# Performance work log

Measured on AMD Instinct MI355X. Metric: run time of the kernel, lower is better.

The kernel has to match this reference:

```python
import jax, jax.numpy as jnp
import numpy as np

B, S, D, H = 4, 2048, 1024, 16  # batch, seq, n_embd, n_head
HD = D // H  # head size = 64


def setup_inputs() -> dict:
    key = jax.random.key(0)
    ks = jax.random.split(key, 5)
    s = 0.02
    return {
        "x": jax.random.normal(ks[0], (B, S, D), dtype=jnp.float32),
        "W_attn": jax.random.normal(ks[1], (D, 3 * D), dtype=jnp.float32) * s,
        "b_attn": jnp.zeros((3 * D,), dtype=jnp.float32),
        "W_proj": jax.random.normal(ks[2], (D, D), dtype=jnp.float32) * s,
        "b_proj": jnp.zeros((D,), dtype=jnp.float32),
    }


def reference(x, W_attn, b_attn, W_proj, b_proj):
    Bx, Sx, Dx = x.shape
    qkv = x @ W_attn + b_attn  # [B,S,3D]
    q, k, v = jnp.split(qkv, 3, axis=-1)
    # [B,H,S,hd]
    q = q.reshape(Bx, Sx, H, HD).transpose(0, 2, 1, 3)
    k = k.reshape(Bx, Sx, H, HD).transpose(0, 2, 1, 3)
    v = v.reshape(Bx, Sx, H, HD).transpose(0, 2, 1, 3)
    scale = 1.0 / jnp.sqrt(jnp.asarray(HD, dtype=x.dtype))
    att = jnp.einsum("bhqd,bhkd->bhqk", q, k) * scale  # [B,H,S,S]
    causal = jnp.tril(jnp.ones((Sx, Sx), dtype=bool))
    att = jnp.where(causal[None, None, :, :], att, jnp.asarray(-jnp.inf, dtype=att.dtype))
    att = jax.nn.softmax(att, axis=-1)
    y = jnp.einsum("bhqk,bhkd->bhqd", att, v)  # [B,H,S,hd]
    y = y.transpose(0, 2, 1, 3).reshape(Bx, Sx, Dx)
    return y @ W_proj + b_proj
```

## Files before the change

kernel.cpp:

```cpp
#include <hip/hip_runtime.h>
#include <math.h>

#define SEQ 2048
#define DIM 1024
#define NH 16
#define HD 64
#define QKV_LD 3072

typedef __attribute__((ext_vector_type(8))) __bf16 bf16x8;
typedef __attribute__((ext_vector_type(8))) unsigned short u16x8;
typedef __attribute__((ext_vector_type(4))) unsigned short u16x4;
typedef __attribute__((ext_vector_type(4))) float f32x4;

typedef unsigned int __attribute__((may_alias)) u32a;

__device__ __forceinline__ unsigned short f2b(float f) {
  unsigned int b = __builtin_bit_cast(unsigned int, f);
  return (unsigned short)((b + 0x7fffu + ((b >> 16) & 1u)) >> 16);
}

__device__ __forceinline__ void gload_lds16(const void* g, void* l) {
  __builtin_amdgcn_global_load_lds((const __attribute__((address_space(1))) void*)g,
                                   (__attribute__((address_space(3))) void*)l,
                                   16, 0, 0);
}

__device__ __forceinline__ bf16x8 ld_frag16(const unsigned short* p) {
  bf16x8 r;
  __builtin_memcpy(&r, __builtin_assume_aligned((void*)p, 16), 16);
  return r;
}

#define BARRIER_VM4()  asm volatile("s_waitcnt vmcnt(4)\ns_barrier" ::: "memory")
#define BARRIER_VM6()  asm volatile("s_waitcnt vmcnt(6)\ns_barrier" ::: "memory")
#define BARRIER_LGKM() asm volatile("s_waitcnt lgkmcnt(0)\ns_barrier" ::: "memory")
#define PH_BAR()       asm volatile("s_barrier" ::: "memory")
#define LGKM0()        asm volatile("s_waitcnt lgkmcnt(0)" ::: "memory")
#define ISSUE_FENCE()  asm volatile("" ::: "memory")


__device__ __forceinline__ void transpose_tile_256(
    const float* __restrict__ W, unsigned short* __restrict__ WT,
    int K, int N, int bx, int by, int tid) {
  __shared__ float tile[32][33];
  const int n0 = bx * 32, k0 = by * 32;
  const int tx = tid & 31, ty0 = tid >> 5;
#pragma unroll
  for (int r = 0; r < 4; ++r)
    tile[ty0 + r * 8][tx] = W[(size_t)(k0 + ty0 + r * 8) * N + n0 + tx];
  __syncthreads();
#pragma unroll
  for (int r = 0; r < 4; ++r)
    WT[(size_t)(n0 + ty0 + r * 8) * K + k0 + tx] = f2b(tile[tx][ty0 + r * 8]);
}

__global__ __launch_bounds__(256) void prep_kernel(
    const float* __restrict__ x, unsigned short* __restrict__ xb, int n,
    const float* __restrict__ Wa, unsigned short* __restrict__ WaT,
    const float* __restrict__ Wp, unsigned short* __restrict__ WpT) {
  const int bid = blockIdx.x;
  const int tid = threadIdx.x;
  if (bid < 8192) {
    const int i = (bid * 256 + tid) * 4;
    if (i >= n) return;
    float4 v = *(const float4*)(x + i);
    u16x4 o;
    o.x = f2b(v.x); o.y = f2b(v.y); o.z = f2b(v.z); o.w = f2b(v.w);
    *(u16x4*)(xb + i) = o;
  } else if (bid < 8192 + 3072) {
    const int t = bid - 8192;
    transpose_tile_256(Wa, WaT, DIM, 3 * DIM, t % 96, t / 96, tid);
  } else {
    const int t = bid - (8192 + 3072);
    transpose_tile_256(Wp, WpT, DIM, DIM, t % 32, t / 32, tid);
  }
}


template <int OUT_F32>
__global__ __launch_bounds__(512, 2) void gemm_bt_v4_kernel(
    const unsigned short* __restrict__ A,
    const unsigned short* __restrict__ BT,
    const float* __restrict__ bias,
    void* __restrict__ C, int M, int N, int K,
    int scale_cols, float scale_val) {
  __shared__ __align__(16) unsigned short As[3][256 * 64];
  __shared__ __align__(16) unsigned short Bs[3][128 * 64];

  const int tid = threadIdx.x;
  const int wave = tid >> 6;
  const int lane = tid & 63;
  const int quad = lane >> 4;
  const int l16 = lane & 15;
  const int r7 = l16 & 7;
  const int m0 = blockIdx.y * 256;
  const int n0 = blockIdx.x * 128;
  const int wm = (wave >> 1) * 64;
  const int wn = (wave & 1) * 64;

  const int srow = tid >> 3;
  const int sg = (tid & 7) ^ (srow & 7);
  const size_t a_gb = (size_t)(m0 + srow) * K + sg * 8;
  const size_t b_gb = (size_t)(n0 + srow) * K + sg * 8;

  f32x4 acc[4][4] = {};
  const int NT = K >> 6;

#define G_STAGE_A(kt_, buf_, j_)                                               \
  gload_lds16(A + a_gb + (size_t)(j_) * 64 * K + (size_t)(kt_) * 64,           \
              &As[buf_][(j_) * 4096 + wave * 512])
#define G_STAGE_B(kt_, buf_, j_)                                               \
  gload_lds16(BT + b_gb + (size_t)(j_) * 64 * K + (size_t)(kt_) * 64,          \
              &Bs[buf_][(j_) * 4096 + wave * 512])
#define G_STAGE_ALL(kt_, buf_)                                                 \
  {                                                                            \
    G_STAGE_A(kt_, buf_, 0); G_STAGE_A(kt_, buf_, 1);                          \
    G_STAGE_A(kt_, buf_, 2); G_STAGE_A(kt_, buf_, 3);                          \
    G_STAGE_B(kt_, buf_, 0); G_STAGE_B(kt_, buf_, 1);                          \
  }

#define V4_PHASE(kk_, la_, lb_, STAGES_, BAR_)                                 \
  {                                                                            \
    const int colg = ((((kk_) << 2) | quad) ^ r7) << 3;                        \
    bf16x8 af[4], bfr[4];                                                      \
    _Pragma("unroll") for (int i = 0; i < 4; ++i)                              \
      af[i] = ld_frag16(&(la_)[(wm + i * 16 + l16) * 64 + colg]);              \
    _Pragma("unroll") for (int i = 0; i < 4; ++i)                              \
      bfr[i] = ld_frag16(&(lb_)[(wn + i * 16 + l16) * 64 + colg]);             \
    STAGES_;                                                                   \
    BAR_;                                                                      \
    LGKM0();                                                                   \
    __builtin_amdgcn_s_setprio(1);                                             \
    _Pragma("unroll") for (int ni = 0; ni < 4; ++ni)                           \
      _Pragma("unroll") for (int mi = 0; mi < 4; ++mi)                         \
        acc[mi][ni] = __builtin_amdgcn_mfma_f32_16x16x32_bf16(                 \
            af[mi], bfr[ni], acc[mi][ni], 0, 0, 0);                            \
    __builtin_amdgcn_s_setprio(0);                                             \
    PH_BAR();                                                                  \
  }

  G_STAGE_ALL(0, 0);
  ISSUE_FENCE();
  G_STAGE_ALL(1, 1);
  BARRIER_VM6();

  for (int t = 0; t < NT; ++t) {
    const int pf = (t + 2 < NT) ? t + 2 : NT - 1;
    const int pb = (t + 2) % 3;
    const unsigned short* la = As[t % 3];
    const unsigned short* lb = Bs[t % 3];
    V4_PHASE(0, la, lb,
             { G_STAGE_A(pf, pb, 0); G_STAGE_A(pf, pb, 1); G_STAGE_B(pf, pb, 0); },
             PH_BAR());
    V4_PHASE(1, la, lb,
             { G_STAGE_A(pf, pb, 2); G_STAGE_A(pf, pb, 3); G_STAGE_B(pf, pb, 1); },
             BARRIER_VM6());
  }

#pragma unroll
  for (int mi = 0; mi < 4; ++mi) {
#pragma unroll
    for (int ni = 0; ni < 4; ++ni) {
      const int col = n0 + wn + ni * 16 + l16;
      const int row = m0 + wm + mi * 16 + quad * 4;
      const float bv = bias[col];
      const float sv = (col < scale_cols) ? scale_val : 1.0f;
#pragma unroll
      for (int r = 0; r < 4; ++r) {
        float v = (acc[mi][ni][r] + bv) * sv;
        if (OUT_F32)
          ((float*)C)[(size_t)(row + r) * N + col] = v;
        else
          ((unsigned short*)C)[(size_t)(row + r) * N + col] = f2b(v);
      }
    }
  }
}


#define FA_PREFETCH(g_, via_, vib_)                                            \
  {                                                                            \
    const int _g = (g_);                                                       \
    const int _tg = (_g < kt) ? _g : 0;                                        \
    const unsigned short* _kg =                                                \
        base + (size_t)(_tg * 64 + ktok_l) * QKV_LD + DIM + h * HD + kchunk * 8; \
    gload_lds16(_kg, &Ks[_g % 3][0][w * 512]);                                 \
    gload_lds16(_kg + 32, &Ks[_g % 3][1][w * 512]);                            \
    const unsigned short* _vg =                                                \
        base + (size_t)(_tg * 64 + 2 * vk) * QKV_LD + 2 * DIM + h * HD + vc;   \
    via_ = *(const u16x8*)_vg;                                                 \
    vib_ = *(const u16x8*)(_vg + QKV_LD);                                      \
  }

#define VT_WRITE(va_, vb_)                                                     \
  {                                                                            \
    u32a* _V32 = (u32a*)Vt;                                                    \
    _Pragma("unroll") for (int j = 0; j < 8; ++j)                              \
      _V32[vwidx[j]] = (unsigned int)(va_)[j] | ((unsigned int)(vb_)[j] << 16);\
  }

#define FA_COMPUTE(i_, t_, kt_, qf_)                                           \
  {                                                                            \
    const unsigned short* _kb0 = &Ks[(i_) % 3][0][0];                          \
    const unsigned short* _kb1 = &Ks[(i_) % 3][1][0];                          \
    bf16x8 kf0[4], kf1[4], vf0[4], vf1[4];                                     \
    _Pragma("unroll") for (int ni = 0; ni < 4; ++ni) {                         \
      const int ro = (ni * 16 + l16) * 32 + ((quad ^ rsw) * 8);                \
      kf0[ni] = ld_frag16(_kb0 + ro);                                          \
      kf1[ni] = ld_frag16(_kb1 + ro);                                          \
      vf0[ni] = ld_frag16(&Vt[quad * 512 + vroff[ni]]);                        \
      vf1[ni] = ld_frag16(&Vt[(4 + quad) * 512 + vroff[ni]]);                  \
    }                                                                          \
    const int qloc = w * 16 + quad * 4;                                        \
    __builtin_amdgcn_s_setprio(1);                                             \
    _Pragma("unroll") for (int m = 0; m < 2; ++m) {                            \
      if (!(m == 0 && (t_) == (kt_)-1)) {   \
        const bool diag = ((t_) == (kt_)-2 + m);                               \
        _Pragma("unroll") for (int ni = 0; ni < 4; ++ni) {                     \
          f32x4 a = {};                                                        \
          a = __builtin_amdgcn_mfma_f32_16x16x32_bf16(qf_[m][0], kf0[ni], a, 0, 0, 0); \
          a = __builtin_amdgcn_mfma_f32_16x16x32_bf16(qf_[m][1], kf1[ni], a, 0, 0, 0); \
          const int kloc = ni * 16 + l16;                                      \
          _Pragma("unroll") for (int r = 0; r < 4; ++r) {                      \
            float p = __builtin_amdgcn_exp2f(a[r]);                            \
            if (diag && kloc > qloc + r) p = 0.0f;                 \
            Ps[w][(quad * 4 + r) * 72 + kloc] =                                \
                (unsigned short)(__builtin_bit_cast(unsigned int, p) >> 16);   \
          }                                                                    \
        }                                                                      \
        _Pragma("unroll") for (int c = 0; c < 2; ++c) {                        \
          const bf16x8 pa = ld_frag16(&Ps[w][l16 * 72 + c * 32 + quad * 8]);   \
          _Pragma("unroll") for (int ni = 0; ni < 4; ++ni)                     \
            o[m][ni] = __builtin_amdgcn_mfma_f32_16x16x32_bf16(                \
                pa, c ? vf1[ni] : vf0[ni], o[m][ni], 0, 0, 0);                 \
          lacc[m] = __builtin_amdgcn_mfma_f32_16x16x32_bf16(pa, onesb,         \
                                                            lacc[m], 0, 0, 0);\
        }                                                                      \
      }                                                                        \
    }                                                                          \
    __builtin_amdgcn_s_setprio(0);                                             \
  }

#define FA_ITER(i_, t_, kt_, qf_, pva, pvb, cva, cvb)                          \
  {                                                                            \
    FA_PREFETCH((i_) + 2, pva, pvb);                                           \
    FA_COMPUTE(i_, t_, kt_, qf_);                                              \
    BARRIER_VM4();                                                             \
    if ((i_) + 1 < (kt_)) {                                                    \
      VT_WRITE(cva, cvb);                                                      \
      BARRIER_LGKM();                                                          \
    }                                                                          \
  }

#define FA_EPILOGUE(q0_)                                                       \
  _Pragma("unroll") for (int m = 0; m < 2; ++m)                                \
  _Pragma("unroll") for (int r = 0; r < 4; ++r) {                              \
    const float lv = __shfl(lacc[m][r], quad << 4);                            \
    const float inv = 1.0f / lv;                                               \
    const int row = (q0_) + m * 64 + w * 16 + quad * 4 + r;                    \
    unsigned short* dst = yatt + (size_t)(b * SEQ + row) * DIM + h * HD + l16; \
    _Pragma("unroll") for (int ni = 0; ni < 4; ++ni)                           \
      dst[ni * 16] = f2b(o[m][ni][r] * inv);                                   \
  }

__global__ __launch_bounds__(256, 2) void flash_kernel(
    const unsigned short* __restrict__ qkv,
    unsigned short* __restrict__ yatt) {
  __shared__ unsigned short Ks[3][2][64 * 32];
  __shared__ __align__(16) unsigned short Vt[8 * 64 * 8];
  __shared__ __align__(16) unsigned short Ps[4][16 * 72];

  const int tid = threadIdx.x;
  const int w = tid >> 6;
  const int lane = tid & 63;
  const int quad = lane >> 4;
  const int l16 = lane & 15;

  const int bid = (int)blockIdx.x;
  const int qt = 15 - (bid >> 6);
  const int bh = bid & 63;
  const int b = bh >> 4;
  const int h = bh & 15;
  const int kt = 2 * qt + 2;
  const int q0 = qt * 128;

  const unsigned short* base = qkv + (size_t)b * SEQ * QKV_LD;

  const int ktok_l = w * 16 + (lane >> 2);
  const int ksw = (ktok_l ^ (ktok_l >> 2)) & 3;
  const int kchunk = (lane & 3) ^ ksw;
  const int rsw = (l16 ^ (l16 >> 2)) & 3;

  const int vk = tid >> 3;
  const int vc = (tid & 7) * 8;
  int vwidx[8];
#pragma unroll
  for (int j = 0; j < 8; ++j)
    vwidx[j] = (vk >> 2) * 256 + (vc | ((j + (vc >> 3)) & 7)) * 4 + (vk & 3);
  int vroff[4];
#pragma unroll
  for (int ni = 0; ni < 4; ++ni) {
    const int dim = ni * 16 + l16;
    vroff[ni] = ((dim & 56) | ((dim + (dim >> 3)) & 7)) * 8;
  }

  u16x8 ob = {};
  if (l16 == 0) {
#pragma unroll
    for (int j = 0; j < 8; ++j) ob[j] = 0x3F80;
  }
  const bf16x8 onesb = __builtin_bit_cast(bf16x8, ob);

  bf16x8 qf[2][2];
#pragma unroll
  for (int m = 0; m < 2; ++m) {
    const unsigned short* qa =
        base + (size_t)(q0 + m * 64 + w * 16 + l16) * QKV_LD + h * HD + quad * 8;
    qf[m][0] = *(const bf16x8*)qa;
    qf[m][1] = *(const bf16x8*)(qa + 32);
  }

  u16x8 va0, vb0, va1, vb1;
  ISSUE_FENCE();
  FA_PREFETCH(0, va0, vb0);
  ISSUE_FENCE();
  FA_PREFETCH(1, va1, vb1);
  BARRIER_VM4();
  VT_WRITE(va0, vb0);
  BARRIER_LGKM();

  f32x4 o[2][4] = {};
  f32x4 lacc[2] = {};

  for (int i = 0; i < kt; i += 2) {
    FA_ITER(i,     i,     kt, qf, va0, vb0, va1, vb1);
    FA_ITER(i + 1, i + 1, kt, qf, va1, vb1, va0, vb0);
  }
  FA_EPILOGUE(q0);
}


extern "C" void kernel_launch(void* const* d_in, const int* in_sizes, int n_in,
                              void* d_out, int out_size, void* d_ws, size_t ws_size,
                              hipStream_t stream) {
  const float* x  = (const float*)d_in[0];
  const float* Wa = (const float*)d_in[1];
  const float* ba = (const float*)d_in[2];
  const float* Wp = (const float*)d_in[3];
  const float* bp = (const float*)d_in[4];
  float* out = (float*)d_out;

  char* ws = (char*)d_ws;
  unsigned short* xb   = (unsigned short*)ws;
  unsigned short* WaT  = (unsigned short*)(ws + 16777216);
  unsigned short* WpT  = (unsigned short*)(ws + 23068672);
  unsigned short* qkv  = (unsigned short*)(ws + 25165824);
  unsigned short* yatt = (unsigned short*)(ws + 75497472);

  const int M = 4 * SEQ;
  const float qscale = 0.125f * 1.44269504089f;

  prep_kernel<<<12288, 256, 0, stream>>>(x, xb, M * DIM, Wa, WaT, Wp, WpT);

  gemm_bt_v4_kernel<0><<<dim3(24, 32), 512, 0, stream>>>(xb, WaT, ba, qkv, M, 3 * DIM, DIM,
                                                         DIM, qscale);

  flash_kernel<<<dim3(1024), 256, 0, stream>>>(qkv, yatt);

  gemm_bt_v4_kernel<1><<<dim3(8, 32), 512, 0, stream>>>(yatt, WpT, bp, out, M, DIM, DIM,
                                                        0, 1.0f);
}
```

Measured before the change: 248.6 us.

## Add 256x256-tile double-buffered GEMM for QKV projection

Adds a new bf16 MFMA GEMM kernel using 256x256 output tiles (each wave computing 128x64) with a two-stage LDS double buffer fed by direct global-to-LDS loads, in place of the previous three-stage 128-column-tile kernel. It is used only for the QKV projection, cutting that launch from 768 to 384 blocks. The larger tile raises arithmetic intensity and reduces global traffic per FLOP. In exchange it uses 128KB of LDS per block and more accumulator registers, which lowers occupancy and leaves fewer blocks than the GPU has CUs, so the load may be uneven.

```diff
diff --git a/kernel.cpp b/kernel.cpp
--- a/kernel.cpp
+++ b/kernel.cpp
@@ -33,6 +33,7 @@
 
 #define BARRIER_VM4()  asm volatile("s_waitcnt vmcnt(4)\ns_barrier" ::: "memory")
 #define BARRIER_VM6()  asm volatile("s_waitcnt vmcnt(6)\ns_barrier" ::: "memory")
+#define BARRIER_VM8()  asm volatile("s_waitcnt vmcnt(8)\ns_barrier" ::: "memory")
 #define BARRIER_LGKM() asm volatile("s_waitcnt lgkmcnt(0)\ns_barrier" ::: "memory")
 #define PH_BAR()       asm volatile("s_barrier" ::: "memory")
 #define LGKM0()        asm volatile("s_waitcnt lgkmcnt(0)" ::: "memory")
@@ -159,6 +160,101 @@
 
 #pragma unroll
   for (int mi = 0; mi < 4; ++mi) {
+#pragma unroll
+    for (int ni = 0; ni < 4; ++ni) {
+      const int col = n0 + wn + ni * 16 + l16;
+      const int row = m0 + wm + mi * 16 + quad * 4;
+      const float bv = bias[col];
+      const float sv = (col < scale_cols) ? scale_val : 1.0f;
+#pragma unroll
+      for (int r = 0; r < 4; ++r) {
+        float v = (acc[mi][ni][r] + bv) * sv;
+        if (OUT_F32)
+          ((float*)C)[(size_t)(row + r) * N + col] = v;
+        else
+          ((unsigned short*)C)[(size_t)(row + r) * N + col] = f2b(v);
+      }
+    }
+  }
+}
+
+
+template <int OUT_F32>
+__global__ __launch_bounds__(512, 2) void gemm_bt_v5_kernel(
+    const unsigned short* __restrict__ A,
+    const unsigned short* __restrict__ BT,
+    const float* __restrict__ bias,
+    void* __restrict__ C, int M, int N, int K,
+    int scale_cols, float scale_val) {
+  __shared__ __align__(16) unsigned short As[2][256 * 64];
+  __shared__ __align__(16) unsigned short Bs[2][256 * 64];
+
+  const int tid = threadIdx.x;
+  const int wave = tid >> 6;
+  const int lane = tid & 63;
+  const int quad = lane >> 4;
+  const int l16 = lane & 15;
+  const int r7 = l16 & 7;
+  const int m0 = blockIdx.y * 256;
+  const int n0 = blockIdx.x * 256;
+  const int wm = (wave >> 2) * 128;
+  const int wn = (wave & 3) * 64;
+
+  const int srow = tid >> 3;
+  const int sg = (tid & 7) ^ (srow & 7);
+  const size_t a_gb = (size_t)(m0 + srow) * K + sg * 8;
+  const size_t b_gb = (size_t)(n0 + srow) * K + sg * 8;
+
+  f32x4 acc[8][4] = {};
+  const int NT = K >> 6;
+
+#define V5_STAGE(kt_, buf_)                                                    \
+  {                                                                            \
+    const size_t _k0 = (size_t)(kt_) * 64;                                     \
+    gload_lds16(A + a_gb + (size_t)0 * 64 * K + _k0, &As[buf_][0 * 4096 + wave * 512]); \
+    gload_lds16(A + a_gb + (size_t)1 * 64 * K + _k0, &As[buf_][1 * 4096 + wave * 512]); \
+    gload_lds16(A + a_gb + (size_t)2 * 64 * K + _k0, &As[buf_][2 * 4096 + wave * 512]); \
+    gload_lds16(A + a_gb + (size_t)3 * 64 * K + _k0, &As[buf_][3 * 4096 + wave * 512]); \
+    gload_lds16(BT + b_gb + (size_t)0 * 64 * K + _k0, &Bs[buf_][0 * 4096 + wave * 512]); \
+    gload_lds16(BT + b_gb + (size_t)1 * 64 * K + _k0, &Bs[buf_][1 * 4096 + wave * 512]); \
+    gload_lds16(BT + b_gb + (size_t)2 * 64 * K + _k0, &Bs[buf_][2 * 4096 + wave * 512]); \
+    gload_lds16(BT + b_gb + (size_t)3 * 64 * K + _k0, &Bs[buf_][3 * 4096 + wave * 512]); \
+  }
+
+  V5_STAGE(0, 0);
+  ISSUE_FENCE();
+
+  for (int t = 0; t < NT; ++t) {
+    const int pf = (t + 1 < NT) ? t + 1 : NT - 1;
+    V5_STAGE(pf, (t + 1) & 1);
+    BARRIER_VM8();
+
+    const unsigned short* la = As[t & 1];
+    const unsigned short* lb = Bs[t & 1];
+#pragma unroll
+    for (int kk = 0; kk < 2; ++kk) {
+      const int colg = (((kk << 2) | quad) ^ r7) << 3;
+      bf16x8 af[8], bfr[4];
+#pragma unroll
+      for (int i = 0; i < 8; ++i)
+        af[i] = ld_frag16(&la[(wm + i * 16 + l16) * 64 + colg]);
+#pragma unroll
+      for (int i = 0; i < 4; ++i)
+        bfr[i] = ld_frag16(&lb[(wn + i * 16 + l16) * 64 + colg]);
+      __builtin_amdgcn_s_setprio(1);
+#pragma unroll
+      for (int ni = 0; ni < 4; ++ni)
+#pragma unroll
+        for (int mi = 0; mi < 8; ++mi)
+          acc[mi][ni] = __builtin_amdgcn_mfma_f32_16x16x32_bf16(
+              af[mi], bfr[ni], acc[mi][ni], 0, 0, 0);
+      __builtin_amdgcn_s_setprio(0);
+    }
+    BARRIER_LGKM();
+  }
+
+#pragma unroll
+  for (int mi = 0; mi < 8; ++mi) {
 #pragma unroll
     for (int ni = 0; ni < 4; ++ni) {
       const int col = n0 + wn + ni * 16 + l16;
@@ -362,7 +458,7 @@
 
   prep_kernel<<<12288, 256, 0, stream>>>(x, xb, M * DIM, Wa, WaT, Wp, WpT);
 
-  gemm_bt_v4_kernel<0><<<dim3(24, 32), 512, 0, stream>>>(xb, WaT, ba, qkv, M, 3 * DIM, DIM,
+  gemm_bt_v5_kernel<0><<<dim3(12, 32), 512, 0, stream>>>(xb, WaT, ba, qkv, M, 3 * DIM, DIM,
                                                          DIM, qscale);
 
   flash_kernel<<<dim3(1024), 256, 0, stream>>>(qkv, yatt);
```

After: 256.4 us. 3.1% more time.
